# Performance work log

Hardware: AMD Instinct MI355X
Metric: run time of the kernel (lower is better)

## Reference

```python
import jax, jax.numpy as jnp
import numpy as np

N_LEVELS = 16
F = 2                      # n_features_per_level
LOG2_HASHMAP = 19
TABLE_SIZE = 1 << LOG2_HASHMAP
BASE_RES = 16.0
FINEST_RES = 512.0
BOX_MIN, BOX_MAX = -1.0, 1.0
PRIMES = jnp.array([1, 2654435761, 805459861], dtype=jnp.uint32)
# corner offsets, i outer / k inner, matching BOX_OFFSETS_3D ordering
OFFSETS = jnp.array([[i, j, k] for i in (0, 1) for j in (0, 1) for k in (0, 1)], dtype=jnp.int32)  # [8,3]


def _hash(coords):
    # coords: int32 [N,8,3]; torch int32 mul wraps mod 2^32 -> emulate with uint32
    c = coords.astype(jnp.uint32)
    h = (c[..., 0] * PRIMES[0]) ^ (c[..., 1] * PRIMES[1]) ^ (c[..., 2] * PRIMES[2])
    return (h & jnp.uint32(TABLE_SIZE - 1)).astype(jnp.int32)


def setup_inputs() -> dict:
    key = jax.random.key(0)
    k1, k2 = jax.random.split(key)
    x = jax.random.uniform(k1, (1_000_000, 3), dtype=jnp.float32) * 2.0 - 1.0  # inside [-1,1]^3
    # nn.init.uniform_(w, -1e-4, 1e-4)
    tables = (jax.random.uniform(k2, (N_LEVELS, TABLE_SIZE, F), dtype=jnp.float32) * 2.0 - 1.0) * 1e-4
    return {"x": x, "tables": tables}


def reference(x, tables):
    n = x.shape[0]
    b = jnp.exp((jnp.log(FINEST_RES) - jnp.log(BASE_RES)) / (N_LEVELS - 1))
    resolutions = jnp.floor(BASE_RES * b ** jnp.arange(N_LEVELS, dtype=jnp.float32))  # [L]
    xc = jnp.clip(x, BOX_MIN, BOX_MAX)

    def level(res, table):
        grid = (BOX_MAX - BOX_MIN) / res                      # scalar
        bl = jnp.floor((xc - BOX_MIN) / grid).astype(jnp.int32)  # [N,3] bottom-left voxel idx
        vmin = bl.astype(jnp.float32) * grid + BOX_MIN        # [N,3]
        idx = bl[:, None, :] + OFFSETS                        # [N,8,3]
        emb = table[_hash(idx)]                               # [N,8,F] irregular gather
        # weights use original (unclamped) x, as in the torch forward
        w = (x - vmin) / grid                                 # [N,3]
        e = emb.reshape(n, 2, 2, 2, F)
        e = e[:, 0] * (1 - w[:, 0, None, None, None]) + e[:, 1] * w[:, 0, None, None, None]  # [N,2,2,F]
        e = e[:, 0] * (1 - w[:, 1, None, None]) + e[:, 1] * w[:, 1, None, None]              # [N,2,F]
        e = e[:, 0] * (1 - w[:, 2, None]) + e[:, 1] * w[:, 2, None]                          # [N,F]
        return e

    out = jax.vmap(level)(resolutions, tables)  # [L,N,F]
    # torch.cat(x_embedded_all, dim=-1): level-major feature layout
    return jnp.transpose(out, (1, 0, 2)).reshape(n, N_LEVELS * F)
```

## Files before the change

### kernel.cpp

```cpp
#include <hip/hip_runtime.h>
#include <cmath>

#define NL 16
#define NCOARSE 6
#define NFINE 10
#define TABLE_SIZE (1u << 19)
#define TABLE_MASK (TABLE_SIZE - 1u)
#define P1 2654435761u
#define P2 805459861u

typedef float f2v __attribute__((ext_vector_type(2)));
typedef float f4v __attribute__((ext_vector_type(4)));
typedef unsigned long long u64;

struct GridParams { float g[NL]; };

__device__ __forceinline__ f2v ld_agent(const f2v* p) {
  u64 raw = __hip_atomic_load((const u64*)p, __ATOMIC_RELAXED, __HIP_MEMORY_SCOPE_AGENT);
  union { u64 u; f2v f; } c; c.u = raw; return c.f;
}

struct Corners { unsigned idx[8]; float wx, wy, wz; };

__device__ __forceinline__ Corners make_corners(
    float g, float px, float py, float pz, float qx, float qy, float qz)
{
  Corners c;
  const float fx = floorf((qx + 1.f) / g);
  const float fy = floorf((qy + 1.f) / g);
  const float fz = floorf((qz + 1.f) / g);
  c.wx = (px - (fx * g - 1.f)) / g;
  c.wy = (py - (fy * g - 1.f)) / g;
  c.wz = (pz - (fz * g - 1.f)) / g;
  const unsigned hx0 = (unsigned)(int)fx;
  const unsigned hy0 = (unsigned)(int)fy * P1;
  const unsigned hz0 = (unsigned)(int)fz * P2;
  const unsigned hx1 = hx0 + 1u;
  const unsigned hy1 = hy0 + P1;
  const unsigned hz1 = hz0 + P2;
  c.idx[0] = (hx0 ^ hy0 ^ hz0) & TABLE_MASK;
  c.idx[1] = (hx0 ^ hy0 ^ hz1) & TABLE_MASK;
  c.idx[2] = (hx0 ^ hy1 ^ hz0) & TABLE_MASK;
  c.idx[3] = (hx0 ^ hy1 ^ hz1) & TABLE_MASK;
  c.idx[4] = (hx1 ^ hy0 ^ hz0) & TABLE_MASK;
  c.idx[5] = (hx1 ^ hy0 ^ hz1) & TABLE_MASK;
  c.idx[6] = (hx1 ^ hy1 ^ hz0) & TABLE_MASK;
  c.idx[7] = (hx1 ^ hy1 ^ hz1) & TABLE_MASK;
  return c;
}

__device__ __forceinline__ f2v trilerp(const f2v e[8], float wx, float wy, float wz) {
  const float ux = 1.f - wx;
  const f2v a00 = e[0] * ux + e[4] * wx;
  const f2v a01 = e[1] * ux + e[5] * wx;
  const f2v a10 = e[2] * ux + e[6] * wx;
  const f2v a11 = e[3] * ux + e[7] * wx;
  const float uy = 1.f - wy;
  const f2v b0 = a00 * uy + a10 * wy;
  const f2v b1 = a01 * uy + a11 * wy;
  const float uz = 1.f - wz;
  return b0 * uz + b1 * wz;
}

__global__ __launch_bounds__(256) void fine_pass_kernel(
    const float* __restrict__ xin, const f2v* __restrict__ tab,
    f2v* __restrict__ wsl, int npts, int strideT, float g)
{
  const int n0 = blockIdx.x * 256 + threadIdx.x;
  const int n1 = n0 + strideT;
  const int c0 = n0 < npts ? n0 : npts - 1;
  const int c1 = n1 < npts ? n1 : npts - 1;

  const float px0 = xin[3 * c0 + 0], py0 = xin[3 * c0 + 1], pz0 = xin[3 * c0 + 2];
  const float px1 = xin[3 * c1 + 0], py1 = xin[3 * c1 + 1], pz1 = xin[3 * c1 + 2];
  const float qx0 = fminf(fmaxf(px0, -1.f), 1.f), qy0 = fminf(fmaxf(py0, -1.f), 1.f), qz0 = fminf(fmaxf(pz0, -1.f), 1.f);
  const float qx1 = fminf(fmaxf(px1, -1.f), 1.f), qy1 = fminf(fmaxf(py1, -1.f), 1.f), qz1 = fminf(fmaxf(pz1, -1.f), 1.f);

  const Corners ca = make_corners(g, px0, py0, pz0, qx0, qy0, qz0);
  const Corners cb = make_corners(g, px1, py1, pz1, qx1, qy1, qz1);

  f2v ea[8], eb[8];
#pragma unroll
  for (int j = 0; j < 8; ++j) ea[j] = ld_agent(tab + ca.idx[j]);
#pragma unroll
  for (int j = 0; j < 8; ++j) eb[j] = ld_agent(tab + cb.idx[j]);

  const f2v ra = trilerp(ea, ca.wx, ca.wy, ca.wz);
  const f2v rb = trilerp(eb, cb.wx, cb.wy, cb.wz);

  if (n0 < npts) __builtin_nontemporal_store(ra, wsl + n0);
  if (n1 < npts) __builtin_nontemporal_store(rb, wsl + n1);
}

__global__ __launch_bounds__(256) void finalize_kernel(
    const float* __restrict__ xin, const float* __restrict__ tables,
    const f2v* __restrict__ ws, float* __restrict__ out, int npts, GridParams gp)
{
  __shared__ f2v lds[NL][257];
  const int t = threadIdx.x;
  const int base = blockIdx.x * 256;
  const int n = base + t;

  if (n < npts) {
    const float px = xin[3 * n + 0], py = xin[3 * n + 1], pz = xin[3 * n + 2];
    const float qx = fminf(fmaxf(px, -1.f), 1.f);
    const float qy = fminf(fmaxf(py, -1.f), 1.f);
    const float qz = fminf(fmaxf(pz, -1.f), 1.f);
#pragma unroll
    for (int l = 0; l < NCOARSE; ++l) {
      const Corners c = make_corners(gp.g[l], px, py, pz, qx, qy, qz);
      const f2v* tab = (const f2v*)tables + (size_t)l * TABLE_SIZE;
      f2v e[8];
#pragma unroll
      for (int j = 0; j < 8; ++j) e[j] = tab[c.idx[j]];
      lds[l][t] = trilerp(e, c.wx, c.wy, c.wz);
    }
#pragma unroll
    for (int li = 0; li < NFINE; ++li)
      lds[NCOARSE + li][t] = __builtin_nontemporal_load(ws + (size_t)li * npts + n);
  }
  __syncthreads();

#pragma unroll
  for (int k = 0; k < 8; ++k) {
    const int j4 = t + 256 * k;
    const int p  = j4 >> 3;
    const int lp = j4 & 7;
    if (base + p < npts) {
      const f2v a = lds[2 * lp + 0][p];
      const f2v b = lds[2 * lp + 1][p];
      const f4v v = { a[0], a[1], b[0], b[1] };
      __builtin_nontemporal_store(v, (f4v*)(out + (size_t)base * 32) + j4);
    }
  }
}

__global__ __launch_bounds__(256) void hash_embed_fused_kernel(
    const float* __restrict__ xin, const float* __restrict__ tables,
    float* __restrict__ out, int npts, GridParams gp)
{
  int n = blockIdx.x * blockDim.x + threadIdx.x;
  if (n >= npts) return;
  const float px = xin[3 * n + 0], py = xin[3 * n + 1], pz = xin[3 * n + 2];
  const float qx = fminf(fmaxf(px, -1.f), 1.f);
  const float qy = fminf(fmaxf(py, -1.f), 1.f);
  const float qz = fminf(fmaxf(pz, -1.f), 1.f);
  f2v acc[NL];
#pragma unroll
  for (int l = 0; l < NL; ++l) {
    const Corners c = make_corners(gp.g[l], px, py, pz, qx, qy, qz);
    const f2v* tab = (const f2v*)tables + (size_t)l * TABLE_SIZE;
    f2v e[8];
#pragma unroll
    for (int j = 0; j < 8; ++j) e[j] = tab[c.idx[j]];
    acc[l] = trilerp(e, c.wx, c.wy, c.wz);
  }
  f4v* o = (f4v*)(out + (size_t)n * 32);
#pragma unroll
  for (int i = 0; i < 8; ++i) {
    f4v v = { acc[2 * i][0], acc[2 * i][1], acc[2 * i + 1][0], acc[2 * i + 1][1] };
    o[i] = v;
  }
}

extern "C" void kernel_launch(void* const* d_in, const int* in_sizes, int n_in,
                              void* d_out, int out_size, void* d_ws, size_t ws_size,
                              hipStream_t stream) {
  const float* x = (const float*)d_in[0];
  const float* tables = (const float*)d_in[1];
  float* out = (float*)d_out;
  const int npts = in_sizes[0] / 3;

  GridParams gp;
  {
    const float b = expf((logf(512.0f) - logf(16.0f)) / 15.0f);
    for (int l = 0; l < NL; ++l) {
      const float r = floorf(16.0f * powf(b, (float)l));
      gp.g[l] = 2.0f / r;
    }
  }

  const size_t ws_needed = (size_t)NFINE * npts * sizeof(f2v);
  if (ws_size >= ws_needed) {
    f2v* ws = (f2v*)d_ws;
    const int gridF = (npts + 511) / 512;
    const int strideT = gridF * 256;
    for (int l = NCOARSE; l < NL; ++l) {
      const f2v* tab = (const f2v*)tables + (size_t)l * TABLE_SIZE;
      f2v* wsl = ws + (size_t)(l - NCOARSE) * npts;
      hipLaunchKernelGGL(fine_pass_kernel, dim3(gridF), dim3(256), 0, stream,
                         x, tab, wsl, npts, strideT, gp.g[l]);
    }
    const int gridZ = (npts + 255) / 256;
    hipLaunchKernelGGL(finalize_kernel, dim3(gridZ), dim3(256), 0, stream,
                       x, tables, ws, out, npts, gp);
  } else {
    const int grid = (npts + 255) / 256;
    hipLaunchKernelGGL(hash_embed_fused_kernel, dim3(grid), dim3(256), 0, stream,
                       x, tables, out, npts, gp);
  }
}
```

Baseline: 542.9 us.

## Pre-rehash coarse levels into dense z-pair grids and restructure level passes

Adds a rehash kernel that expands the hashed tables of the seven coarsest levels into dense voxel grids, storing z-adjacent corner pairs together as float4 and using the output buffer as scratch. Coarse levels then need four 16-byte loads per point instead of eight scattered 8-byte hash gathers. Fine levels now process four points per thread to raise memory-level parallelism. All levels write to the workspace and a separate transpose kernel builds the output. The trade-off is the per-call cost of the rehash kernel plus a full workspace round trip for every level, and the path relies on the output buffer being large enough to hold the pair grids.

New measurement: 520.4 us. -4.2%, faster.

```diff
diff --git a/kernel.cpp b/kernel.cpp
--- a/kernel.cpp
+++ b/kernel.cpp
@@ -2,8 +2,7 @@
 #include <cmath>
 
 #define NL 16
-#define NCOARSE 6
-#define NFINE 10
+#define NPAIR 7
 #define TABLE_SIZE (1u << 19)
 #define TABLE_MASK (TABLE_SIZE - 1u)
 #define P1 2654435761u
@@ -13,7 +12,13 @@
 typedef float f4v __attribute__((ext_vector_type(4)));
 typedef unsigned long long u64;
 
-struct GridParams { float g[NL]; };
+struct Params {
+  float g[NL];
+  int R[NPAIR];
+  unsigned off[NPAIR];
+  unsigned nE[NPAIR];
+  unsigned totE;
+};
 
 __device__ __forceinline__ f2v ld_agent(const f2v* p) {
   u64 raw = __hip_atomic_load((const u64*)p, __ATOMIC_RELAXED, __HIP_MEMORY_SCOPE_AGENT);
@@ -62,69 +67,141 @@
   return b0 * uz + b1 * wz;
 }
 
-__global__ __launch_bounds__(256) void fine_pass_kernel(
-    const float* __restrict__ xin, const f2v* __restrict__ tab,
-    f2v* __restrict__ wsl, int npts, int strideT, float g)
+__device__ __forceinline__ f2v pair_eval(
+    const f4v* __restrict__ pt, int R, float g,
+    float px, float py, float pz, float qx, float qy, float qz)
+{
+  const float fx = floorf((qx + 1.f) / g);
+  const float fy = floorf((qy + 1.f) / g);
+  const float fz = floorf((qz + 1.f) / g);
+  const float wx = (px - (fx * g - 1.f)) / g;
+  const float wy = (py - (fy * g - 1.f)) / g;
+  const float wz = (pz - (fz * g - 1.f)) / g;
+  const int bx = (int)fx, by = (int)fy, bz = (int)fz;
+  const int s = R + 1;
+  const int base = (bx * (R + 2) + by) * s + bz;
+  const f4v p00 = pt[base];
+  const f4v p01 = pt[base + s];
+  const f4v p10 = pt[base + (R + 2) * s];
+  const f4v p11 = pt[base + (R + 3) * s];
+  const float uz = 1.f - wz;
+  const f2v a00 = { p00[0] * uz + p00[2] * wz, p00[1] * uz + p00[3] * wz };
+  const f2v a01 = { p01[0] * uz + p01[2] * wz, p01[1] * uz + p01[3] * wz };
+  const f2v a10 = { p10[0] * uz + p10[2] * wz, p10[1] * uz + p10[3] * wz };
+  const f2v a11 = { p11[0] * uz + p11[2] * wz, p11[1] * uz + p11[3] * wz };
+  const float uy = 1.f - wy;
+  const f2v b0 = a00 * uy + a01 * wy;
+  const f2v b1 = a10 * uy + a11 * wy;
+  const float ux = 1.f - wx;
+  return b0 * ux + b1 * wx;
+}
+
+__global__ __launch_bounds__(256) void rehash_kernel(
+    const float* __restrict__ tables, f4v* __restrict__ pt, Params P)
+{
+  unsigned tid = blockIdx.x * 256 + threadIdx.x;
+  if (tid >= P.totE) return;
+  int l = 0; unsigned e = tid;
+  while (e >= P.nE[l]) { e -= P.nE[l]; ++l; }
+  const unsigned R = (unsigned)P.R[l];
+  const unsigned vz = e % (R + 1u);
+  const unsigned t2 = e / (R + 1u);
+  const unsigned vy = t2 % (R + 2u);
+  const unsigned vx = t2 / (R + 2u);
+  const f2v* tab = (const f2v*)tables + (size_t)l * TABLE_SIZE;
+  const unsigned h0 = (vx ^ (vy * P1) ^ (vz * P2)) & TABLE_MASK;
+  const unsigned h1 = (vx ^ (vy * P1) ^ ((vz + 1u) * P2)) & TABLE_MASK;
+  const f2v a = tab[h0], b = tab[h1];
+  const f4v o = { a[0], a[1], b[0], b[1] };
+  pt[P.off[l] + e] = o;
+}
+
+__global__ __launch_bounds__(256) void coarse_pass_kernel(
+    const float* __restrict__ xin, const f4v* __restrict__ pt,
+    f2v* __restrict__ ws, int npts, Params P)
+{
+  const int n = blockIdx.x * 256 + threadIdx.x;
+  if (n >= npts) return;
+  const float px = __builtin_nontemporal_load(&xin[3 * n + 0]);
+  const float py = __builtin_nontemporal_load(&xin[3 * n + 1]);
+  const float pz = __builtin_nontemporal_load(&xin[3 * n + 2]);
+  const float qx = fminf(fmaxf(px, -1.f), 1.f);
+  const float qy = fminf(fmaxf(py, -1.f), 1.f);
+  const float qz = fminf(fmaxf(pz, -1.f), 1.f);
+#pragma unroll
+  for (int l = 0; l < 5; ++l) {
+    const f2v r = pair_eval(pt + P.off[l], P.R[l], P.g[l], px, py, pz, qx, qy, qz);
+    __builtin_nontemporal_store(r, ws + (size_t)l * npts + n);
+  }
+}
+
+__global__ __launch_bounds__(256) void pair_pass_kernel(
+    const float* __restrict__ xin, const f4v* __restrict__ pt,
+    f2v* __restrict__ wsl, int npts, int strideT, int R, float g)
 {
   const int n0 = blockIdx.x * 256 + threadIdx.x;
   const int n1 = n0 + strideT;
   const int c0 = n0 < npts ? n0 : npts - 1;
   const int c1 = n1 < npts ? n1 : npts - 1;
-
   const float px0 = xin[3 * c0 + 0], py0 = xin[3 * c0 + 1], pz0 = xin[3 * c0 + 2];
   const float px1 = xin[3 * c1 + 0], py1 = xin[3 * c1 + 1], pz1 = xin[3 * c1 + 2];
   const float qx0 = fminf(fmaxf(px0, -1.f), 1.f), qy0 = fminf(fmaxf(py0, -1.f), 1.f), qz0 = fminf(fmaxf(pz0, -1.f), 1.f);
   const float qx1 = fminf(fmaxf(px1, -1.f), 1.f), qy1 = fminf(fmaxf(py1, -1.f), 1.f), qz1 = fminf(fmaxf(pz1, -1.f), 1.f);
-
-  const Corners ca = make_corners(g, px0, py0, pz0, qx0, qy0, qz0);
-  const Corners cb = make_corners(g, px1, py1, pz1, qx1, qy1, qz1);
-
-  f2v ea[8], eb[8];
-#pragma unroll
-  for (int j = 0; j < 8; ++j) ea[j] = ld_agent(tab + ca.idx[j]);
-#pragma unroll
-  for (int j = 0; j < 8; ++j) eb[j] = ld_agent(tab + cb.idx[j]);
-
-  const f2v ra = trilerp(ea, ca.wx, ca.wy, ca.wz);
-  const f2v rb = trilerp(eb, cb.wx, cb.wy, cb.wz);
-
-  if (n0 < npts) __builtin_nontemporal_store(ra, wsl + n0);
-  if (n1 < npts) __builtin_nontemporal_store(rb, wsl + n1);
-}
-
-__global__ __launch_bounds__(256) void finalize_kernel(
-    const float* __restrict__ xin, const float* __restrict__ tables,
-    const f2v* __restrict__ ws, float* __restrict__ out, int npts, GridParams gp)
+  const f2v r0 = pair_eval(pt, R, g, px0, py0, pz0, qx0, qy0, qz0);
+  const f2v r1 = pair_eval(pt, R, g, px1, py1, pz1, qx1, qy1, qz1);
+  if (n0 < npts) __builtin_nontemporal_store(r0, wsl + n0);
+  if (n1 < npts) __builtin_nontemporal_store(r1, wsl + n1);
+}
+
+__global__ __launch_bounds__(256) void fine_pass_kernel(
+    const float* __restrict__ xin, const f2v* __restrict__ tab,
+    f2v* __restrict__ wsl, int npts, int strideT, float g)
+{
+  const int nb = blockIdx.x * 256 + threadIdx.x;
+  int n[4], c[4];
+#pragma unroll
+  for (int i = 0; i < 4; ++i) {
+    n[i] = nb + i * strideT;
+    c[i] = n[i] < npts ? n[i] : npts - 1;
+  }
+  Corners cr[4];
+#pragma unroll
+  for (int i = 0; i < 4; ++i) {
+    const float px = xin[3 * c[i] + 0], py = xin[3 * c[i] + 1], pz = xin[3 * c[i] + 2];
+    const float qx = fminf(fmaxf(px, -1.f), 1.f);
+    const float qy = fminf(fmaxf(py, -1.f), 1.f);
+    const float qz = fminf(fmaxf(pz, -1.f), 1.f);
+    cr[i] = make_corners(g, px, py, pz, qx, qy, qz);
+  }
+  f2v e[4][8];
+#pragma unroll
+  for (int i = 0; i < 4; ++i)
+#pragma unroll
+    for (int j = 0; j < 8; ++j) e[i][j] = ld_agent(tab + cr[i].idx[j]);
+#pragma unroll
+  for (int i = 0; i < 4; ++i) {
+    const f2v r = trilerp(e[i], cr[i].wx, cr[i].wy, cr[i].wz);
+    if (n[i] < npts) __builtin_nontemporal_store(r, wsl + n[i]);
+  }
+}
+
+__global__ __launch_bounds__(256) void transpose_kernel(
+    const f2v* __restrict__ ws, float* __restrict__ out, int npts)
 {
   __shared__ f2v lds[NL][257];
   const int t = threadIdx.x;
   const int base = blockIdx.x * 256;
   const int n = base + t;
-
   if (n < npts) {
-    const float px = xin[3 * n + 0], py = xin[3 * n + 1], pz = xin[3 * n + 2];
-    const float qx = fminf(fmaxf(px, -1.f), 1.f);
-    const float qy = fminf(fmaxf(py, -1.f), 1.f);
-    const float qz = fminf(fmaxf(pz, -1.f), 1.f);
-#pragma unroll
-    for (int l = 0; l < NCOARSE; ++l) {
-      const Corners c = make_corners(gp.g[l], px, py, pz, qx, qy, qz);
-      const f2v* tab = (const f2v*)tables + (size_t)l * TABLE_SIZE;
-      f2v e[8];
-#pragma unroll
-      for (int j = 0; j < 8; ++j) e[j] = tab[c.idx[j]];
-      lds[l][t] = trilerp(e, c.wx, c.wy, c.wz);
-    }
-#pragma unroll
-    for (int li = 0; li < NFINE; ++li)
-      lds[NCOARSE + li][t] = __builtin_nontemporal_load(ws + (size_t)li * npts + n);
+#pragma unroll
+    for (int l = 0; l < NL; ++l)
+      lds[l][t] = __builtin_nontemporal_load(ws + (size_t)l * npts + n);
   }
   __syncthreads();
-
 #pragma unroll
   for (int k = 0; k < 8; ++k) {
     const int j4 = t + 256 * k;
-    const int p  = j4 >> 3;
+    const int p = j4 >> 3;
     const int lp = j4 & 7;
     if (base + p < npts) {
       const f2v a = lds[2 * lp + 0][p];
@@ -137,7 +214,7 @@
 
 __global__ __launch_bounds__(256) void hash_embed_fused_kernel(
     const float* __restrict__ xin, const float* __restrict__ tables,
-    float* __restrict__ out, int npts, GridParams gp)
+    float* __restrict__ out, int npts, Params P)
 {
   int n = blockIdx.x * blockDim.x + threadIdx.x;
   if (n >= npts) return;
@@ -148,7 +225,7 @@
   f2v acc[NL];
 #pragma unroll
   for (int l = 0; l < NL; ++l) {
-    const Corners c = make_corners(gp.g[l], px, py, pz, qx, qy, qz);
+    const Corners c = make_corners(P.g[l], px, py, pz, qx, qy, qz);
     const f2v* tab = (const f2v*)tables + (size_t)l * TABLE_SIZE;
     f2v e[8];
 #pragma unroll
@@ -158,7 +235,7 @@
   f4v* o = (f4v*)(out + (size_t)n * 32);
 #pragma unroll
   for (int i = 0; i < 8; ++i) {
-    f4v v = { acc[2 * i][0], acc[2 * i][1], acc[2 * i + 1][0], acc[2 * i + 1][1] };
+    const f4v v = { acc[2 * i][0], acc[2 * i][1], acc[2 * i + 1][0], acc[2 * i + 1][1] };
     o[i] = v;
   }
 }
@@ -171,32 +248,56 @@
   float* out = (float*)d_out;
   const int npts = in_sizes[0] / 3;
 
-  GridParams gp;
+  Params P;
   {
     const float b = expf((logf(512.0f) - logf(16.0f)) / 15.0f);
+    unsigned off = 0;
     for (int l = 0; l < NL; ++l) {
       const float r = floorf(16.0f * powf(b, (float)l));
-      gp.g[l] = 2.0f / r;
+      P.g[l] = 2.0f / r;
+      if (l < NPAIR) {
+        const int R = (int)r;
+        P.R[l] = R;
+        P.nE[l] = (unsigned)((R + 2) * (R + 2) * (R + 1));
+        P.off[l] = off;
+        off += P.nE[l];
+      }
     }
-  }
-
-  const size_t ws_needed = (size_t)NFINE * npts * sizeof(f2v);
-  if (ws_size >= ws_needed) {
+    P.totE = off;
+  }
+
+  const size_t ws_needed = (size_t)NL * npts * sizeof(f2v);
+  const size_t pair_bytes = (size_t)P.totE * sizeof(f4v);
+  const size_t out_bytes = (size_t)out_size * sizeof(float);
+
+  if (ws_size >= ws_needed && out_bytes >= pair_bytes) {
     f2v* ws = (f2v*)d_ws;
-    const int gridF = (npts + 511) / 512;
-    const int strideT = gridF * 256;
-    for (int l = NCOARSE; l < NL; ++l) {
-      const f2v* tab = (const f2v*)tables + (size_t)l * TABLE_SIZE;
-      f2v* wsl = ws + (size_t)(l - NCOARSE) * npts;
-      hipLaunchKernelGGL(fine_pass_kernel, dim3(gridF), dim3(256), 0, stream,
-                         x, tab, wsl, npts, strideT, gp.g[l]);
-    }
-    const int gridZ = (npts + 255) / 256;
-    hipLaunchKernelGGL(finalize_kernel, dim3(gridZ), dim3(256), 0, stream,
-                       x, tables, ws, out, npts, gp);
+    f4v* pt = (f4v*)d_out;
+
+    hipLaunchKernelGGL(rehash_kernel, dim3((P.totE + 255) / 256), dim3(256), 0, stream,
+                       tables, pt, P);
+
+    hipLaunchKernelGGL(coarse_pass_kernel, dim3((npts + 255) / 256), dim3(256), 0, stream,
+                       x, pt, ws, npts, P);
+
+    const int grid2 = (npts + 511) / 512;
+    const int stride2 = grid2 * 256;
+    for (int l = 5; l < NPAIR; ++l)
+      hipLaunchKernelGGL(pair_pass_kernel, dim3(grid2), dim3(256), 0, stream,
+                         x, pt + P.off[l], ws + (size_t)l * npts, npts, stride2,
+                         P.R[l], P.g[l]);
+
+    const int grid4 = (npts + 1023) / 1024;
+    const int stride4 = grid4 * 256;
+    for (int l = NPAIR; l < NL; ++l)
+      hipLaunchKernelGGL(fine_pass_kernel, dim3(grid4), dim3(256), 0, stream,
+                         x, (const f2v*)tables + (size_t)l * TABLE_SIZE,
+                         ws + (size_t)l * npts, npts, stride4, P.g[l]);
+
+    hipLaunchKernelGGL(transpose_kernel, dim3((npts + 255) / 256), dim3(256), 0, stream,
+                       ws, out, npts);
   } else {
-    const int grid = (npts + 255) / 256;
-    hipLaunchKernelGGL(hash_embed_fused_kernel, dim3(grid), dim3(256), 0, stream,
-                       x, tables, out, npts, gp);
-  }
-}
+    hipLaunchKernelGGL(hash_embed_fused_kernel, dim3((npts + 255) / 256), dim3(256), 0, stream,
+                       x, tables, out, npts, P);
+  }
+}
```
